# Kernel tuning notes

Measured on AMD Instinct MI355X. Metric: run time of the kernel, lower is better.

## Reference

```python
import jax, jax.numpy as jnp
import numpy as np

B, N, K, H = 8, 2048, 30, 128
SCALE = 30.0
EPS = 1e-5


def _gelu(x):
    return jax.nn.gelu(x, approximate=False)


def _lin(x, w, b):
    return x @ w.T + b


def _ln(x, g, b):
    m = x.mean(-1, keepdims=True)
    v = ((x - m) ** 2).mean(-1, keepdims=True)
    return g * (x - m) * jax.lax.rsqrt(v + EPS) + b


def _gather_nodes(h_V, E_idx):
    # h_V: [B,N,H], E_idx: [B,N,K] -> [B,N,K,H]
    b_idx = jnp.arange(h_V.shape[0])[:, None, None]
    return h_V[b_idx, E_idx]


def setup_inputs() -> dict:
    key = jax.random.key(0)
    ks = jax.random.split(key, 16)
    p = 0.02
    inp = {
        'h_V': jax.random.normal(ks[0], (B, N, H), jnp.float32),
        'h_E': jax.random.normal(ks[1], (B, N, K, H), jnp.float32),
        'E_idx': jax.random.randint(ks[2], (B, N, K), 0, N, jnp.int32),
        'mask_V': jnp.ones((B, N), jnp.float32),
        'mask_attend': jnp.ones((B, N, K), jnp.float32),
        # node message MLP (3H -> H -> H -> H)
        'W1_w': jax.random.normal(ks[3], (H, 3 * H), jnp.float32) * p,
        'W1_b': jnp.zeros((H,), jnp.float32),
        'W2_w': jax.random.normal(ks[4], (H, H), jnp.float32) * p,
        'W2_b': jnp.zeros((H,), jnp.float32),
        'W3_w': jax.random.normal(ks[5], (H, H), jnp.float32) * p,
        'W3_b': jnp.zeros((H,), jnp.float32),
        # edge message MLP (3H -> H -> H -> H)
        'W11_w': jax.random.normal(ks[6], (H, 3 * H), jnp.float32) * p,
        'W11_b': jnp.zeros((H,), jnp.float32),
        'W12_w': jax.random.normal(ks[7], (H, H), jnp.float32) * p,
        'W12_b': jnp.zeros((H,), jnp.float32),
        'W13_w': jax.random.normal(ks[8], (H, H), jnp.float32) * p,
        'W13_b': jnp.zeros((H,), jnp.float32),
        # layer norms
        'n1_g': jnp.ones((H,), jnp.float32), 'n1_b': jnp.zeros((H,), jnp.float32),
        'n2_g': jnp.ones((H,), jnp.float32), 'n2_b': jnp.zeros((H,), jnp.float32),
        'n3_g': jnp.ones((H,), jnp.float32), 'n3_b': jnp.zeros((H,), jnp.float32),
        # position-wise FFN (H -> 4H -> H)
        'din_w': jax.random.normal(ks[9], (4 * H, H), jnp.float32) * p,
        'din_b': jnp.zeros((4 * H,), jnp.float32),
        'dout_w': jax.random.normal(ks[10], (H, 4 * H), jnp.float32) * p,
        'dout_b': jnp.zeros((H,), jnp.float32),
    }
    return inp


def reference(h_V, h_E, E_idx, mask_V, mask_attend,
              W1_w, W1_b, W2_w, W2_b, W3_w, W3_b,
              W11_w, W11_b, W12_w, W12_b, W13_w, W13_b,
              n1_g, n1_b, n2_g, n2_b, n3_g, n3_b,
              din_w, din_b, dout_w, dout_b):
    k = h_E.shape[-2]
    # --- node update ---
    h_nbr = _gather_nodes(h_V, E_idx)                       # [B,N,K,H]
    h_V_exp = jnp.broadcast_to(h_V[:, :, None, :], h_nbr.shape)
    h_EV = jnp.concatenate([h_V_exp, h_nbr, h_E], axis=-1)  # [B,N,K,3H]
    h_message = _lin(_gelu(_lin(_gelu(_lin(h_EV, W1_w, W1_b)), W2_w, W2_b)), W3_w, W3_b)
    h_message = mask_attend[..., None] * h_message
    dh = jnp.sum(h_message, axis=-2) / SCALE
    h_V = _ln(h_V + dh, n1_g, n1_b)
    dh = _lin(_gelu(_lin(h_V, din_w, din_b)), dout_w, dout_b)
    h_V = _ln(h_V + dh, n2_g, n2_b)
    h_V = mask_V[..., None] * h_V
    # --- edge update ---
    h_nbr = _gather_nodes(h_V, E_idx)
    h_V_exp = jnp.broadcast_to(h_V[:, :, None, :], h_nbr.shape)
    h_EV = jnp.concatenate([h_V_exp, h_nbr, h_E], axis=-1)
    h_message = _lin(_gelu(_lin(_gelu(_lin(h_EV, W11_w, W11_b)), W12_w, W12_b)), W13_w, W13_b)
    h_E = _ln(h_E + h_message, n3_g, n3_b)
    return (h_V, h_E)
```

## Files before the change

### kernel.cpp

```cpp
#include <hip/hip_runtime.h>

#define B_ 8
#define N_ 2048
#define K_ 30
#define H_ 128
#define LDA 136
#define LDM 132
#define EPS_ 1e-5f

typedef __attribute__((ext_vector_type(8))) short short8;
typedef __attribute__((ext_vector_type(4))) float f32x4;

__device__ inline unsigned pkbf(float lo, float hi) {
  unsigned r;
  asm("v_cvt_pk_bf16_f32 %0, %1, %2" : "=v"(r) : "v"(lo), "v"(hi));
  return r;
}

__device__ inline unsigned short f2bf(float f) { return (unsigned short)pkbf(f, f); }

__device__ inline float bf2f(unsigned short h) {
  union { unsigned u; float f; } v; v.u = ((unsigned)h) << 16; return v.f;
}

__device__ inline float gelu_t(float x) {
  const float p = x * x;
  const float z = x * (1.5957691216057308f + 0.07135481627f * p);
  const float e = exp2f(z * -1.4426950408889634f);
  return x * __builtin_amdgcn_rcpf(1.0f + e);
}

__device__ inline short8 pack8(float4 a, float4 b) {
  union { unsigned u[4]; short8 s; } v;
  v.u[0] = pkbf(a.x, a.y); v.u[1] = pkbf(a.z, a.w);
  v.u[2] = pkbf(b.x, b.y); v.u[3] = pkbf(b.z, b.w);
  return v.s;
}

template<int LDW>
__device__ inline void gemmT(const unsigned short* __restrict__ sA,
                             const unsigned short* __restrict__ W,
                             int lane, int cb, f32x4 (&acc)[4][2]) {
  const int rl = lane & 15;
  const int klo = (lane >> 4) << 3;
#pragma unroll
  for (int ks = 0; ks < 4; ++ks) {
    short8 wf[2];
#pragma unroll
    for (int fn = 0; fn < 2; ++fn)
      wf[fn] = *(const short8*)(W + (size_t)(cb + fn * 16 + rl) * LDW + ks * 32 + klo);
#pragma unroll
    for (int et = 0; et < 4; ++et) {
      const short8 ef = *(const short8*)(sA + (et * 16 + rl) * LDA + ks * 32 + klo);
      acc[et][0] = __builtin_amdgcn_mfma_f32_16x16x32_bf16(wf[0], ef, acc[et][0], 0, 0, 0);
      acc[et][1] = __builtin_amdgcn_mfma_f32_16x16x32_bf16(wf[1], ef, acc[et][1], 0, 0, 0);
    }
  }
}

#define ZERO42(A) \
  _Pragma("unroll") for (int e_ = 0; e_ < 4; ++e_) { A[e_][0] = (f32x4){0,0,0,0}; A[e_][1] = (f32x4){0,0,0,0}; }

template<int LDW, int NN>
__device__ inline void gemm64(const unsigned short* __restrict__ sA,
                              const unsigned short* __restrict__ W,
                              int lane, int cb, f32x4 (&acc)[4][NN]) {
  const int rl = lane & 15;
  const int klo = (lane >> 4) << 3;
#pragma unroll
  for (int ks = 0; ks < 4; ++ks) {
    short8 a[4];
#pragma unroll
    for (int m = 0; m < 4; ++m)
      a[m] = *(const short8*)(sA + (m * 16 + rl) * LDA + ks * 32 + klo);
#pragma unroll
    for (int n = 0; n < NN; ++n) {
      const short8 b8 = *(const short8*)(W + (size_t)(cb + n * 16 + rl) * LDW + ks * 32 + klo);
#pragma unroll
      for (int m = 0; m < 4; ++m)
        acc[m][n] = __builtin_amdgcn_mfma_f32_16x16x32_bf16(a[m], b8, acc[m][n], 0, 0, 0);
    }
  }
}

__global__ __launch_bounds__(256) void prep(const float* __restrict__ w1, const float* __restrict__ w2,
                                            const float* __restrict__ w3, const float* __restrict__ w11,
                                            const float* __restrict__ w12, const float* __restrict__ w13,
                                            const float* __restrict__ din, const float* __restrict__ dout,
                                            unsigned short* __restrict__ dst) {
  const int i = blockIdx.x * 256 + threadIdx.x;
  const float* s; int off;
  if (i < 49152)       { s = w1;  off = 0; }
  else if (i < 65536)  { s = w2;  off = 49152; }
  else if (i < 81920)  { s = w3;  off = 65536; }
  else if (i < 131072) { s = w11; off = 81920; }
  else if (i < 147456) { s = w12; off = 131072; }
  else if (i < 163840) { s = w13; off = 147456; }
  else if (i < 229376) { s = din; off = 163840; }
  else                 { s = dout; off = 229376; }
  dst[i] = f2bf(s[i - off]);
}

template<bool F32SRC, bool SPLIT>
__global__ __launch_bounds__(256) void preY(const void* __restrict__ Xv,
                                            const unsigned short* __restrict__ Wbase,
                                            unsigned short* __restrict__ Yc,
                                            unsigned short* __restrict__ Yn) {
  __shared__ __align__(16) unsigned short sA[64 * LDA];
  const int tid = threadIdx.x;
  const int lane = tid & 63;
  const int w = tid >> 6;
  const int rows = blockIdx.x << 6;
  const int rl = lane & 15;
  const int h4 = (lane >> 4) << 2;

  if (F32SRC) {
    const float* X = (const float*)Xv;
    for (int t = tid; t < 1024; t += 256) {
      const int r = t >> 4, seg = t & 15;
      const float* src = X + (((size_t)(rows + r)) << 7) + seg * 8;
      *(short8*)(sA + r * LDA + seg * 8) = pack8(*(const float4*)src, *(const float4*)(src + 4));
    }
  } else {
    const unsigned short* X = (const unsigned short*)Xv;
    for (int t = tid; t < 1024; t += 256) {
      const int r = t >> 4, seg = t & 15;
      *(short8*)(sA + r * LDA + seg * 8) =
          *(const short8*)(X + (((size_t)(rows + r)) << 7) + seg * 8);
    }
  }
  __syncthreads();

  const int half = w >> 1;
  const int cb = (w & 1) * 64;
  f32x4 acc[4][4];
#pragma unroll
  for (int m = 0; m < 4; ++m)
#pragma unroll
    for (int n = 0; n < 4; ++n) acc[m][n] = (f32x4){0, 0, 0, 0};
  gemm64<384, 4>(sA, Wbase + half * 128, lane, cb, acc);

  unsigned short* Y = half ? Yn : Yc;
  const int stride = SPLIT ? 128 : 256;
  const int coff = SPLIT ? 0 : half * 128;
#pragma unroll
  for (int n = 0; n < 4; ++n) {
    const int col = coff + cb + n * 16 + rl;
#pragma unroll
    for (int m = 0; m < 4; ++m)
#pragma unroll
      for (int i = 0; i < 4; ++i)
        Y[(size_t)(rows + m * 16 + h4 + i) * stride + col] = f2bf(acc[m][n][i]);
  }
}

__global__ __launch_bounds__(256, 4) void k1(
    const float* __restrict__ hV, const float* __restrict__ hE,
    const int* __restrict__ Eidx, const float* __restrict__ mattend,
    const unsigned short* __restrict__ wc, const unsigned short* __restrict__ Y1,
    const float* __restrict__ W1b, const float* __restrict__ W2b,
    const float* __restrict__ W3b, const float* __restrict__ n1g,
    const float* __restrict__ n1b, unsigned short* __restrict__ hV1b,
    float* __restrict__ outE) {
  __shared__ __align__(16) unsigned short sBuf[2 * 64 * LDA];
  __shared__ __align__(16) unsigned short sYc[2 * 128];
  __shared__ float sMask[64];
  __shared__ float sRed[2][128];
  unsigned short* sE = sBuf;
  unsigned short* sG = sBuf + 64 * LDA;
  float* sM = (float*)sBuf;

  const int tid = threadIdx.x;
  const int lane = tid & 63;
  const int w = tid >> 6;
  const int rl = lane & 15;
  const int h4 = (lane >> 4) << 2;
  const int bid = (blockIdx.x & 7) * 1024 + (blockIdx.x >> 3);
  const int v0 = bid << 1;
  const int b = v0 >> 11;
  const int n0 = v0 & (N_ - 1);
  const int bBase = b * N_;

  const unsigned short* W1c = wc;
  const unsigned short* W2c = wc + 49152;
  const unsigned short* W3c = wc + 65536;

  for (int t = tid; t < 1024; t += 256) {
    const int r = t >> 4, seg = t & 15;
    const int g = r >> 5, kk = r & 31;
    const int kc = kk < K_ ? kk : K_ - 1;
    const size_t e = (size_t)(bBase + n0 + g) * K_ + kc;
    const float* src = hE + (e << 7) + seg * 8;
    const short8 o = pack8(*(const float4*)src, *(const float4*)(src + 4));
    *(short8*)(sE + r * LDA + seg * 8) = o;
    if (kk < K_)
      *(short8*)((unsigned short*)(outE + (e << 7)) + 128 + seg * 8) = o;
  }
  for (int t = tid; t < 1024; t += 256) {
    const int r = t >> 4, seg = t & 15;
    const int g = r >> 5;
    int kk = r & 31; if (kk >= K_) kk = K_ - 1;
    const int j = Eidx[(bBase + n0 + g) * K_ + kk];
    *(short8*)(sG + r * LDA + seg * 8) =
        *(const short8*)(Y1 + (size_t)(bBase + j) * 256 + 128 + seg * 8);
  }
  {
    const int g = tid >> 7, c = tid & 127;
    sYc[g * 128 + c] = Y1[(size_t)(bBase + n0 + g) * 256 + c];
  }
  if (tid < 64) {
    const int g = tid >> 5, kk = tid & 31;
    sMask[tid] = (kk < K_) ? mattend[(bBase + n0 + g) * K_ + kk] : 0.f;
  }
  __syncthreads();

  f32x4 acc[4][2];
  ZERO42(acc)
  gemmT<384>(sE, W1c + 256, lane, w * 32, acc);

  {
    float4 b1v[2];
    b1v[0] = *(const float4*)(W1b + w * 32 + h4);
    b1v[1] = *(const float4*)(W1b + w * 32 + 16 + h4);
#pragma unroll
    for (int et = 0; et < 4; ++et) {
      const int e = et * 16 + rl;
      const int g = et >> 1;
#pragma unroll
      for (int fn = 0; fn < 2; ++fn) {
        const int f0 = w * 32 + fn * 16 + h4;
        const ushort4 yc = *(const ushort4*)(sYc + g * 128 + f0);
        const ushort4 yn = *(const ushort4*)(sG + e * LDA + f0);
        const float x0 = gelu_t(acc[et][fn][0] + b1v[fn].x + bf2f(yc.x) + bf2f(yn.x));
        const float x1 = gelu_t(acc[et][fn][1] + b1v[fn].y + bf2f(yc.y) + bf2f(yn.y));
        const float x2 = gelu_t(acc[et][fn][2] + b1v[fn].z + bf2f(yc.z) + bf2f(yn.z));
        const float x3 = gelu_t(acc[et][fn][3] + b1v[fn].w + bf2f(yc.w) + bf2f(yn.w));
        uint2 o; o.x = pkbf(x0, x1); o.y = pkbf(x2, x3);
        *(uint2*)(sG + e * LDA + f0) = o;
      }
    }
  }
  __syncthreads();

  f32x4 acc2[4][2];
  ZERO42(acc2)
  gemmT<128>(sG, W2c, lane, w * 32, acc2);
  __syncthreads();
  {
    float4 b2v[2];
    b2v[0] = *(const float4*)(W2b + w * 32 + h4);
    b2v[1] = *(const float4*)(W2b + w * 32 + 16 + h4);
#pragma unroll
    for (int et = 0; et < 4; ++et) {
      const int e = et * 16 + rl;
#pragma unroll
      for (int fn = 0; fn < 2; ++fn) {
        const int f0 = w * 32 + fn * 16 + h4;
        const float x0 = gelu_t(acc2[et][fn][0] + b2v[fn].x);
        const float x1 = gelu_t(acc2[et][fn][1] + b2v[fn].y);
        const float x2 = gelu_t(acc2[et][fn][2] + b2v[fn].z);
        const float x3 = gelu_t(acc2[et][fn][3] + b2v[fn].w);
        uint2 o; o.x = pkbf(x0, x1); o.y = pkbf(x2, x3);
        *(uint2*)(sG + e * LDA + f0) = o;
      }
    }
  }
  __syncthreads();

  f32x4 acc3[4][2];
  ZERO42(acc3)
  gemmT<128>(sG, W3c, lane, w * 32, acc3);
  __syncthreads();

  {
    float4 b3v[2];
    b3v[0] = *(const float4*)(W3b + w * 32 + h4);
    b3v[1] = *(const float4*)(W3b + w * 32 + 16 + h4);
#pragma unroll
    for (int et = 0; et < 4; ++et) {
      const int e = et * 16 + rl;
      const float mk = sMask[e];
#pragma unroll
      for (int fn = 0; fn < 2; ++fn) {
        const int f0 = w * 32 + fn * 16 + h4;
        const float4 v = make_float4((acc3[et][fn][0] + b3v[fn].x) * mk,
                                     (acc3[et][fn][1] + b3v[fn].y) * mk,
                                     (acc3[et][fn][2] + b3v[fn].z) * mk,
                                     (acc3[et][fn][3] + b3v[fn].w) * mk);
        *(float4*)(sM + e * LDM + f0) = v;
      }
    }
  }
  __syncthreads();

  {
    const int g = tid >> 7, f = tid & 127;
    float s = 0.f;
#pragma unroll
    for (int kk = 0; kk < 32; ++kk) s += sM[(g * 32 + kk) * LDM + f];
    sRed[g][f] = s;
  }
  __syncthreads();

  if (w < 2) {
    const size_t base = ((size_t)(bBase + n0 + w)) << 7;
    const float x0 = hV[base + lane] + sRed[w][lane] * (1.0f / 30.0f);
    const float x1 = hV[base + 64 + lane] + sRed[w][64 + lane] * (1.0f / 30.0f);
    float s = x0 + x1;
#pragma unroll
    for (int o = 1; o < 64; o <<= 1) s += __shfl_xor(s, o);
    const float mean = s * (1.0f / 128.0f);
    const float d0 = x0 - mean, d1 = x1 - mean;
    float vs = d0 * d0 + d1 * d1;
#pragma unroll
    for (int o = 1; o < 64; o <<= 1) vs += __shfl_xor(vs, o);
    const float inv = rsqrtf(vs * (1.0f / 128.0f) + EPS_);
    hV1b[base + lane] = f2bf(n1g[lane] * (d0 * inv) + n1b[lane]);
    hV1b[base + 64 + lane] = f2bf(n1g[64 + lane] * (d1 * inv) + n1b[64 + lane]);
  }
}

__global__ __launch_bounds__(256) void k2(
    const unsigned short* __restrict__ hV1b, const unsigned short* __restrict__ wc,
    const float* __restrict__ dinb, const float* __restrict__ doutb,
    const float* __restrict__ n2g, const float* __restrict__ n2b,
    const float* __restrict__ maskV, float* __restrict__ outV,
    unsigned short* __restrict__ hV2c) {
  __shared__ __align__(16) unsigned short sT[16 * LDA];
  __shared__ float sStat[16][2][4];

  const int tid = threadIdx.x;
  const int lane = tid & 63;
  const int w = tid >> 6;
  const int rl = lane & 15;
  const int h4 = (lane >> 4) << 2;
  const int klo = (lane >> 4) << 3;
  const int rowbase = blockIdx.x << 4;

  const unsigned short* dinc = wc + 163840;
  const unsigned short* doutc = wc + 229376;

  short8 ef[4];
#pragma unroll
  for (int ks = 0; ks < 4; ++ks)
    ef[ks] = *(const short8*)(hV1b + (((size_t)(rowbase + rl)) << 7) + ks * 32 + klo);

  f32x4 acc2[2];
  acc2[0] = (f32x4){0, 0, 0, 0}; acc2[1] = (f32x4){0, 0, 0, 0};

  for (int c = 0; c < 4; ++c) {
    f32x4 acc1[2];
    acc1[0] = (f32x4){0, 0, 0, 0}; acc1[1] = (f32x4){0, 0, 0, 0};
#pragma unroll
    for (int ks = 0; ks < 4; ++ks)
#pragma unroll
      for (int fn = 0; fn < 2; ++fn) {
        const short8 wf = *(const short8*)(dinc + (size_t)(c * 128 + w * 32 + fn * 16 + rl) * 128 + ks * 32 + klo);
        acc1[fn] = __builtin_amdgcn_mfma_f32_16x16x32_bf16(wf, ef[ks], acc1[fn], 0, 0, 0);
      }
    __syncthreads();
    {
      float4 db[2];
      db[0] = *(const float4*)(dinb + c * 128 + w * 32 + h4);
      db[1] = *(const float4*)(dinb + c * 128 + w * 32 + 16 + h4);
#pragma unroll
      for (int fn = 0; fn < 2; ++fn) {
        const int f0 = w * 32 + fn * 16 + h4;
        const float x0 = gelu_t(acc1[fn][0] + db[fn].x);
        const float x1 = gelu_t(acc1[fn][1] + db[fn].y);
        const float x2 = gelu_t(acc1[fn][2] + db[fn].z);
        const float x3 = gelu_t(acc1[fn][3] + db[fn].w);
        uint2 o; o.x = pkbf(x0, x1); o.y = pkbf(x2, x3);
        *(uint2*)(sT + rl * LDA + f0) = o;
      }
    }
    __syncthreads();
#pragma unroll
    for (int ks = 0; ks < 4; ++ks) {
      const short8 xf = *(const short8*)(sT + rl * LDA + ks * 32 + klo);
#pragma unroll
      for (int fn = 0; fn < 2; ++fn) {
        const short8 wf2 = *(const short8*)(doutc + (size_t)(w * 32 + fn * 16 + rl) * 512 + c * 128 + ks * 32 + klo);
        acc2[fn] = __builtin_amdgcn_mfma_f32_16x16x32_bf16(wf2, xf, acc2[fn], 0, 0, 0);
      }
    }
  }

  const int row = rl;
  const int grow = rowbase + row;
  {
    float4 wbv[2];
    wbv[0] = *(const float4*)(doutb + w * 32 + h4);
    wbv[1] = *(const float4*)(doutb + w * 32 + 16 + h4);
    float s = 0.f, ss = 0.f;
#pragma unroll
    for (int fn = 0; fn < 2; ++fn) {
      const int f0 = w * 32 + fn * 16 + h4;
      const ushort4 rr = *(const ushort4*)(hV1b + (((size_t)grow) << 7) + f0);
      const float x0 = acc2[fn][0] + wbv[fn].x + bf2f(rr.x);
      const float x1 = acc2[fn][1] + wbv[fn].y + bf2f(rr.y);
      const float x2 = acc2[fn][2] + wbv[fn].z + bf2f(rr.z);
      const float x3 = acc2[fn][3] + wbv[fn].w + bf2f(rr.w);
      acc2[fn] = (f32x4){x0, x1, x2, x3};
      s += x0 + x1 + x2 + x3;
      ss += x0 * x0 + x1 * x1 + x2 * x2 + x3 * x3;
    }
    s += __shfl_xor(s, 16); s += __shfl_xor(s, 32);
    ss += __shfl_xor(ss, 16); ss += __shfl_xor(ss, 32);
    if (lane < 16) { sStat[row][0][w] = s; sStat[row][1][w] = ss; }
  }
  __syncthreads();
  {
    const float sum = sStat[row][0][0] + sStat[row][0][1] + sStat[row][0][2] + sStat[row][0][3];
    const float ssq = sStat[row][1][0] + sStat[row][1][1] + sStat[row][1][2] + sStat[row][1][3];
    const float mean = sum * (1.0f / 128.0f);
    const float inv = rsqrtf(ssq * (1.0f / 128.0f) - mean * mean + EPS_);
    const float mv = maskV[grow];
#pragma unroll
    for (int fn = 0; fn < 2; ++fn) {
      const int f0 = w * 32 + fn * 16 + h4;
      const float4 gv = *(const float4*)(n2g + f0);
      const float4 bv = *(const float4*)(n2b + f0);
      const float y0 = (gv.x * (acc2[fn][0] - mean) * inv + bv.x) * mv;
      const float y1 = (gv.y * (acc2[fn][1] - mean) * inv + bv.y) * mv;
      const float y2 = (gv.z * (acc2[fn][2] - mean) * inv + bv.z) * mv;
      const float y3 = (gv.w * (acc2[fn][3] - mean) * inv + bv.w) * mv;
      *(float4*)(outV + (((size_t)grow) << 7) + f0) = make_float4(y0, y1, y2, y3);
      uint2 o; o.x = pkbf(y0, y1); o.y = pkbf(y2, y3);
      *(uint2*)(hV2c + (((size_t)grow) << 7) + f0) = o;
    }
  }
}

__global__ __launch_bounds__(256, 4) void k3(
    const int* __restrict__ Eidx, const unsigned short* __restrict__ wc,
    const unsigned short* __restrict__ Y2c, const unsigned short* __restrict__ Y2n,
    const float* __restrict__ W11b, const float* __restrict__ W12b,
    const float* __restrict__ W13b, const float* __restrict__ n3g,
    const float* __restrict__ n3b, float* __restrict__ outE) {
  __shared__ __align__(16) unsigned short sE[64 * LDA];
  __shared__ __align__(16) unsigned short sG[64 * LDA];
  __shared__ unsigned short sYc[2 * 128];
  __shared__ float sStat[64][2][4];

  const int tid = threadIdx.x;
  const int lane = tid & 63;
  const int w = tid >> 6;
  const int rl = lane & 15;
  const int h4 = (lane >> 4) << 2;
  const int bid = (blockIdx.x & 7) * 1024 + (blockIdx.x >> 3);
  const int v0 = bid << 1;
  const int b = v0 >> 11;
  const int n0 = v0 & (N_ - 1);
  const int bBase = b * N_;

  const unsigned short* W11c = wc + 81920;
  const unsigned short* W12c = wc + 131072;
  const unsigned short* W13c = wc + 147456;

  for (int t = tid; t < 1024; t += 256) {
    const int r = t >> 4, seg = t & 15;
    const int g = r >> 5;
    int kk = r & 31; if (kk >= K_) kk = K_ - 1;
    const size_t e = (size_t)(bBase + n0 + g) * K_ + kk;
    *(short8*)(sE + r * LDA + seg * 8) =
        *(const short8*)((const unsigned short*)(outE + (e << 7)) + 128 + seg * 8);
  }
  for (int t = tid; t < 1024; t += 256) {
    const int r = t >> 4, seg = t & 15;
    const int g = r >> 5;
    int kk = r & 31; if (kk >= K_) kk = K_ - 1;
    const int j = Eidx[(bBase + n0 + g) * K_ + kk];
    *(short8*)(sG + r * LDA + seg * 8) =
        *(const short8*)(Y2n + (size_t)(bBase + j) * 128 + seg * 8);
  }
  {
    const int g = tid >> 7, c = tid & 127;
    sYc[g * 128 + c] = Y2c[(size_t)(bBase + n0 + g) * 128 + c];
  }
  __syncthreads();

  f32x4 acc[4][2];
  ZERO42(acc)
  gemm64<384, 2>(sE, W11c + 256, lane, w * 32, acc);

#pragma unroll
  for (int n = 0; n < 2; ++n) {
    const int f = w * 32 + n * 16 + rl;
    const float bb = W11b[f];
#pragma unroll
    for (int m = 0; m < 4; ++m)
#pragma unroll
      for (int i = 0; i < 4; ++i) {
        const int e = m * 16 + h4 + i;
        const float x = acc[m][n][i] + bb + bf2f(sYc[(e >> 5) * 128 + f]) + bf2f(sG[e * LDA + f]);
        sG[e * LDA + f] = f2bf(gelu_t(x));
      }
  }
  __syncthreads();

  f32x4 acc2[4][2];
  ZERO42(acc2)
  gemm64<128, 2>(sG, W12c, lane, w * 32, acc2);
  __syncthreads();
#pragma unroll
  for (int n = 0; n < 2; ++n) {
    const int f = w * 32 + n * 16 + rl;
    const float bb = W12b[f];
#pragma unroll
    for (int m = 0; m < 4; ++m)
#pragma unroll
      for (int i = 0; i < 4; ++i) {
        const int e = m * 16 + h4 + i;
        sG[e * LDA + f] = f2bf(gelu_t(acc2[m][n][i] + bb));
      }
  }
  __syncthreads();

  f32x4 acc3[4][2];
  ZERO42(acc3)
  gemm64<128, 2>(sG, W13c, lane, w * 32, acc3);

  float gc[2], bc[2], wb[2];
#pragma unroll
  for (int n = 0; n < 2; ++n) {
    const int f = w * 32 + n * 16 + rl;
    gc[n] = n3g[f]; bc[n] = n3b[f]; wb[n] = W13b[f];
  }
#pragma unroll
  for (int m = 0; m < 4; ++m)
#pragma unroll
    for (int i = 0; i < 4; ++i) {
      const int e = m * 16 + h4 + i;
      float s = 0.f, ss = 0.f;
#pragma unroll
      for (int n = 0; n < 2; ++n) {
        const int f = w * 32 + n * 16 + rl;
        const float x = acc3[m][n][i] + wb[n] + bf2f(sE[e * LDA + f]);
        acc3[m][n][i] = x;
        s += x; ss += x * x;
      }
#pragma unroll
      for (int o = 1; o <= 8; o <<= 1) { s += __shfl_xor(s, o); ss += __shfl_xor(ss, o); }
      if (rl == 0) { sStat[e][0][w] = s; sStat[e][1][w] = ss; }
    }
  __syncthreads();
#pragma unroll
  for (int m = 0; m < 4; ++m)
#pragma unroll
    for (int i = 0; i < 4; ++i) {
      const int e = m * 16 + h4 + i;
      const int g = e >> 5, kk = e & 31;
      if (kk >= K_) continue;
      const float sum = sStat[e][0][0] + sStat[e][0][1] + sStat[e][0][2] + sStat[e][0][3];
      const float ssq = sStat[e][1][0] + sStat[e][1][1] + sStat[e][1][2] + sStat[e][1][3];
      const float mean = sum * (1.0f / 128.0f);
      const float inv = rsqrtf(ssq * (1.0f / 128.0f) - mean * mean + EPS_);
      float* dst = outE + (((size_t)((bBase + n0 + g) * K_ + kk)) << 7) + w * 32 + rl;
#pragma unroll
      for (int n = 0; n < 2; ++n)
        dst[n * 16] = gc[n] * (acc3[m][n][i] - mean) * inv + bc[n];
    }
}

extern "C" void kernel_launch(void* const* d_in, const int* in_sizes, int n_in,
                              void* d_out, int out_size, void* d_ws, size_t ws_size,
                              hipStream_t stream) {
  const float* hV = (const float*)d_in[0];
  const float* hE = (const float*)d_in[1];
  const int* Eidx = (const int*)d_in[2];
  const float* maskV = (const float*)d_in[3];
  const float* mattend = (const float*)d_in[4];
  const float* W1w = (const float*)d_in[5];   const float* W1b = (const float*)d_in[6];
  const float* W2w = (const float*)d_in[7];   const float* W2b = (const float*)d_in[8];
  const float* W3w = (const float*)d_in[9];   const float* W3b = (const float*)d_in[10];
  const float* W11w = (const float*)d_in[11]; const float* W11b = (const float*)d_in[12];
  const float* W12w = (const float*)d_in[13]; const float* W12b = (const float*)d_in[14];
  const float* W13w = (const float*)d_in[15]; const float* W13b = (const float*)d_in[16];
  const float* n1g = (const float*)d_in[17];  const float* n1b = (const float*)d_in[18];
  const float* n2g = (const float*)d_in[19];  const float* n2b = (const float*)d_in[20];
  const float* n3g = (const float*)d_in[21];  const float* n3b = (const float*)d_in[22];
  const float* dinw = (const float*)d_in[23]; const float* dinb = (const float*)d_in[24];
  const float* doutw = (const float*)d_in[25]; const float* doutb = (const float*)d_in[26];

  unsigned short* wc   = (unsigned short*)d_ws;
  unsigned short* R1   = wc + 294912;
  unsigned short* R2   = R1 + 4194304;
  unsigned short* Y1   = R1;
  unsigned short* hV1b = R2;
  unsigned short* hV2c = R1;
  unsigned short* Y2c  = R1 + 2097152;
  unsigned short* Y2n  = R2;

  float* outV = (float*)d_out;
  float* outE = outV + (size_t)B_ * N_ * H_;

  prep<<<1152, 256, 0, stream>>>(W1w, W2w, W3w, W11w, W12w, W13w, dinw, doutw, wc);
  preY<true, false><<<256, 256, 0, stream>>>(hV, wc, Y1, Y1);
  k1<<<8192, 256, 0, stream>>>(hV, hE, Eidx, mattend, wc, Y1,
                               W1b, W2b, W3b, n1g, n1b, hV1b, outE);
  k2<<<1024, 256, 0, stream>>>(hV1b, wc, dinb, doutb, n2g, n2b, maskV, outV, hV2c);
  preY<false, true><<<256, 256, 0, stream>>>(hV2c, wc + 81920, Y2c, Y2n);
  k3<<<8192, 256, 0, stream>>>(Eidx, wc, Y2c, Y2n,
                               W11b, W12b, W13b, n3g, n3b, outE);
}
```

Baseline: 457.9 us.

## Process one node per block with two waves in edge MLP kernels

k1 and k3 now handle one node (32 padded edge rows) per 128-thread block instead of two nodes per 256-thread block. Each wave computes 64 output features across 32 rows with new gemmT1/gemm32 tiles, and the LayerNorm and reduction bookkeeping is simplified to match. The aim is to cut shared memory per block and raise the number of resident blocks for better latency hiding. In exchange, each block spends more of its time on fixed setup and barriers, and weight fragments are reused across fewer rows.

After: 570.9 us. +24.7%, slower.

```diff
diff --git a/kernel.cpp b/kernel.cpp
--- a/kernel.cpp
+++ b/kernel.cpp
@@ -38,28 +38,48 @@
 }
 
 template<int LDW>
-__device__ inline void gemmT(const unsigned short* __restrict__ sA,
-                             const unsigned short* __restrict__ W,
-                             int lane, int cb, f32x4 (&acc)[4][2]) {
+__device__ inline void gemmT1(const unsigned short* __restrict__ sA,
+                              const unsigned short* __restrict__ W,
+                              int lane, int cb, f32x4 (&acc)[2][4]) {
   const int rl = lane & 15;
   const int klo = (lane >> 4) << 3;
 #pragma unroll
   for (int ks = 0; ks < 4; ++ks) {
-    short8 wf[2];
-#pragma unroll
-    for (int fn = 0; fn < 2; ++fn)
+    short8 wf[4];
+#pragma unroll
+    for (int fn = 0; fn < 4; ++fn)
       wf[fn] = *(const short8*)(W + (size_t)(cb + fn * 16 + rl) * LDW + ks * 32 + klo);
 #pragma unroll
-    for (int et = 0; et < 4; ++et) {
+    for (int et = 0; et < 2; ++et) {
       const short8 ef = *(const short8*)(sA + (et * 16 + rl) * LDA + ks * 32 + klo);
-      acc[et][0] = __builtin_amdgcn_mfma_f32_16x16x32_bf16(wf[0], ef, acc[et][0], 0, 0, 0);
-      acc[et][1] = __builtin_amdgcn_mfma_f32_16x16x32_bf16(wf[1], ef, acc[et][1], 0, 0, 0);
-    }
-  }
-}
-
-#define ZERO42(A) \
-  _Pragma("unroll") for (int e_ = 0; e_ < 4; ++e_) { A[e_][0] = (f32x4){0,0,0,0}; A[e_][1] = (f32x4){0,0,0,0}; }
+#pragma unroll
+      for (int fn = 0; fn < 4; ++fn)
+        acc[et][fn] = __builtin_amdgcn_mfma_f32_16x16x32_bf16(wf[fn], ef, acc[et][fn], 0, 0, 0);
+    }
+  }
+}
+
+template<int LDW>
+__device__ inline void gemm32(const unsigned short* __restrict__ sA,
+                              const unsigned short* __restrict__ W,
+                              int lane, int cb, f32x4 (&acc)[2][4]) {
+  const int rl = lane & 15;
+  const int klo = (lane >> 4) << 3;
+#pragma unroll
+  for (int ks = 0; ks < 4; ++ks) {
+    short8 a[2];
+#pragma unroll
+    for (int m = 0; m < 2; ++m)
+      a[m] = *(const short8*)(sA + (m * 16 + rl) * LDA + ks * 32 + klo);
+#pragma unroll
+    for (int n = 0; n < 4; ++n) {
+      const short8 b8 = *(const short8*)(W + (size_t)(cb + n * 16 + rl) * LDW + ks * 32 + klo);
+#pragma unroll
+      for (int m = 0; m < 2; ++m)
+        acc[m][n] = __builtin_amdgcn_mfma_f32_16x16x32_bf16(a[m], b8, acc[m][n], 0, 0, 0);
+    }
+  }
+}
 
 template<int LDW, int NN>
 __device__ inline void gemm64(const unsigned short* __restrict__ sA,
@@ -82,6 +102,10 @@
     }
   }
 }
+
+#define ZERO24(A) \
+  _Pragma("unroll") for (int e_ = 0; e_ < 2; ++e_) \
+  _Pragma("unroll") for (int f_ = 0; f_ < 4; ++f_) A[e_][f_] = (f32x4){0.f, 0.f, 0.f, 0.f};
 
 __global__ __launch_bounds__(256) void prep(const float* __restrict__ w1, const float* __restrict__ w2,
                                             const float* __restrict__ w3, const float* __restrict__ w11,
@@ -154,7 +178,7 @@
   }
 }
 
-__global__ __launch_bounds__(256, 4) void k1(
+__global__ __launch_bounds__(128, 4) void k1(
     const float* __restrict__ hV, const float* __restrict__ hE,
     const int* __restrict__ Eidx, const float* __restrict__ mattend,
     const unsigned short* __restrict__ wc, const unsigned short* __restrict__ Y1,
@@ -162,12 +186,12 @@
     const float* __restrict__ W3b, const float* __restrict__ n1g,
     const float* __restrict__ n1b, unsigned short* __restrict__ hV1b,
     float* __restrict__ outE) {
-  __shared__ __align__(16) unsigned short sBuf[2 * 64 * LDA];
-  __shared__ __align__(16) unsigned short sYc[2 * 128];
-  __shared__ float sMask[64];
-  __shared__ float sRed[2][128];
+  __shared__ __align__(16) unsigned short sBuf[2 * 32 * LDA];
+  __shared__ __align__(16) unsigned short sYc[128];
+  __shared__ float sMask[32];
+  __shared__ float sRed[128];
   unsigned short* sE = sBuf;
-  unsigned short* sG = sBuf + 64 * LDA;
+  unsigned short* sG = sBuf + 32 * LDA;
   float* sM = (float*)sBuf;
 
   const int tid = threadIdx.x;
@@ -175,61 +199,52 @@
   const int w = tid >> 6;
   const int rl = lane & 15;
   const int h4 = (lane >> 4) << 2;
-  const int bid = (blockIdx.x & 7) * 1024 + (blockIdx.x >> 3);
-  const int v0 = bid << 1;
-  const int b = v0 >> 11;
-  const int n0 = v0 & (N_ - 1);
+  const int bid = (blockIdx.x & 7) * 2048 + (blockIdx.x >> 3);
+  const int b = bid >> 11;
+  const int n0 = bid & (N_ - 1);
   const int bBase = b * N_;
+  const int node = bBase + n0;
 
   const unsigned short* W1c = wc;
   const unsigned short* W2c = wc + 49152;
   const unsigned short* W3c = wc + 65536;
 
-  for (int t = tid; t < 1024; t += 256) {
+  for (int t = tid; t < 512; t += 128) {
     const int r = t >> 4, seg = t & 15;
-    const int g = r >> 5, kk = r & 31;
-    const int kc = kk < K_ ? kk : K_ - 1;
-    const size_t e = (size_t)(bBase + n0 + g) * K_ + kc;
+    const int kc = r < K_ ? r : K_ - 1;
+    const size_t e = (size_t)node * K_ + kc;
     const float* src = hE + (e << 7) + seg * 8;
     const short8 o = pack8(*(const float4*)src, *(const float4*)(src + 4));
     *(short8*)(sE + r * LDA + seg * 8) = o;
-    if (kk < K_)
+    if (r < K_)
       *(short8*)((unsigned short*)(outE + (e << 7)) + 128 + seg * 8) = o;
   }
-  for (int t = tid; t < 1024; t += 256) {
+  for (int t = tid; t < 512; t += 128) {
     const int r = t >> 4, seg = t & 15;
-    const int g = r >> 5;
-    int kk = r & 31; if (kk >= K_) kk = K_ - 1;
-    const int j = Eidx[(bBase + n0 + g) * K_ + kk];
+    const int kc = r < K_ ? r : K_ - 1;
+    const int j = Eidx[node * K_ + kc];
     *(short8*)(sG + r * LDA + seg * 8) =
         *(const short8*)(Y1 + (size_t)(bBase + j) * 256 + 128 + seg * 8);
   }
+  sYc[tid] = Y1[(size_t)node * 256 + tid];
+  if (tid < 32) sMask[tid] = (tid < K_) ? mattend[node * K_ + tid] : 0.f;
+  __syncthreads();
+
+  f32x4 acc[2][4];
+  ZERO24(acc)
+  gemmT1<384>(sE, W1c + 256, lane, w * 64, acc);
+
   {
-    const int g = tid >> 7, c = tid & 127;
-    sYc[g * 128 + c] = Y1[(size_t)(bBase + n0 + g) * 256 + c];
-  }
-  if (tid < 64) {
-    const int g = tid >> 5, kk = tid & 31;
-    sMask[tid] = (kk < K_) ? mattend[(bBase + n0 + g) * K_ + kk] : 0.f;
-  }
-  __syncthreads();
-
-  f32x4 acc[4][2];
-  ZERO42(acc)
-  gemmT<384>(sE, W1c + 256, lane, w * 32, acc);
-
-  {
-    float4 b1v[2];
-    b1v[0] = *(const float4*)(W1b + w * 32 + h4);
-    b1v[1] = *(const float4*)(W1b + w * 32 + 16 + h4);
-#pragma unroll
-    for (int et = 0; et < 4; ++et) {
+    float4 b1v[4];
+#pragma unroll
+    for (int fn = 0; fn < 4; ++fn) b1v[fn] = *(const float4*)(W1b + w * 64 + fn * 16 + h4);
+#pragma unroll
+    for (int et = 0; et < 2; ++et) {
       const int e = et * 16 + rl;
-      const int g = et >> 1;
-#pragma unroll
-      for (int fn = 0; fn < 2; ++fn) {
-        const int f0 = w * 32 + fn * 16 + h4;
-        const ushort4 yc = *(const ushort4*)(sYc + g * 128 + f0);
+#pragma unroll
+      for (int fn = 0; fn < 4; ++fn) {
+        const int f0 = w * 64 + fn * 16 + h4;
+        const ushort4 yc = *(const ushort4*)(sYc + f0);
         const ushort4 yn = *(const ushort4*)(sG + e * LDA + f0);
         const float x0 = gelu_t(acc[et][fn][0] + b1v[fn].x + bf2f(yc.x) + bf2f(yn.x));
         const float x1 = gelu_t(acc[et][fn][1] + b1v[fn].y + bf2f(yc.y) + bf2f(yn.y));
@@ -242,20 +257,20 @@
   }
   __syncthreads();
 
-  f32x4 acc2[4][2];
-  ZERO42(acc2)
-  gemmT<128>(sG, W2c, lane, w * 32, acc2);
+  f32x4 acc2[2][4];
+  ZERO24(acc2)
+  gemmT1<128>(sG, W2c, lane, w * 64, acc2);
   __syncthreads();
   {
-    float4 b2v[2];
-    b2v[0] = *(const float4*)(W2b + w * 32 + h4);
-    b2v[1] = *(const float4*)(W2b + w * 32 + 16 + h4);
-#pragma unroll
-    for (int et = 0; et < 4; ++et) {
+    float4 b2v[4];
+#pragma unroll
+    for (int fn = 0; fn < 4; ++fn) b2v[fn] = *(const float4*)(W2b + w * 64 + fn * 16 + h4);
+#pragma unroll
+    for (int et = 0; et < 2; ++et) {
       const int e = et * 16 + rl;
 #pragma unroll
-      for (int fn = 0; fn < 2; ++fn) {
-        const int f0 = w * 32 + fn * 16 + h4;
+      for (int fn = 0; fn < 4; ++fn) {
+        const int f0 = w * 64 + fn * 16 + h4;
         const float x0 = gelu_t(acc2[et][fn][0] + b2v[fn].x);
         const float x1 = gelu_t(acc2[et][fn][1] + b2v[fn].y);
         const float x2 = gelu_t(acc2[et][fn][2] + b2v[fn].z);
@@ -267,22 +282,22 @@
   }
   __syncthreads();
 
-  f32x4 acc3[4][2];
-  ZERO42(acc3)
-  gemmT<128>(sG, W3c, lane, w * 32, acc3);
+  f32x4 acc3[2][4];
+  ZERO24(acc3)
+  gemmT1<128>(sG, W3c, lane, w * 64, acc3);
   __syncthreads();
 
   {
-    float4 b3v[2];
-    b3v[0] = *(const float4*)(W3b + w * 32 + h4);
-    b3v[1] = *(const float4*)(W3b + w * 32 + 16 + h4);
-#pragma unroll
-    for (int et = 0; et < 4; ++et) {
+    float4 b3v[4];
+#pragma unroll
+    for (int fn = 0; fn < 4; ++fn) b3v[fn] = *(const float4*)(W3b + w * 64 + fn * 16 + h4);
+#pragma unroll
+    for (int et = 0; et < 2; ++et) {
       const int e = et * 16 + rl;
       const float mk = sMask[e];
 #pragma unroll
-      for (int fn = 0; fn < 2; ++fn) {
-        const int f0 = w * 32 + fn * 16 + h4;
+      for (int fn = 0; fn < 4; ++fn) {
+        const int f0 = w * 64 + fn * 16 + h4;
         const float4 v = make_float4((acc3[et][fn][0] + b3v[fn].x) * mk,
                                      (acc3[et][fn][1] + b3v[fn].y) * mk,
                                      (acc3[et][fn][2] + b3v[fn].z) * mk,
@@ -294,18 +309,17 @@
   __syncthreads();
 
   {
-    const int g = tid >> 7, f = tid & 127;
     float s = 0.f;
 #pragma unroll
-    for (int kk = 0; kk < 32; ++kk) s += sM[(g * 32 + kk) * LDM + f];
-    sRed[g][f] = s;
-  }
-  __syncthreads();
-
-  if (w < 2) {
-    const size_t base = ((size_t)(bBase + n0 + w)) << 7;
-    const float x0 = hV[base + lane] + sRed[w][lane] * (1.0f / 30.0f);
-    const float x1 = hV[base + 64 + lane] + sRed[w][64 + lane] * (1.0f / 30.0f);
+    for (int kk = 0; kk < 32; ++kk) s += sM[kk * LDM + tid];
+    sRed[tid] = s;
+  }
+  __syncthreads();
+
+  if (w == 0) {
+    const size_t base = ((size_t)node) << 7;
+    const float x0 = hV[base + lane] + sRed[lane] * (1.0f / 30.0f);
+    const float x1 = hV[base + 64 + lane] + sRed[64 + lane] * (1.0f / 30.0f);
     float s = x0 + x1;
 #pragma unroll
     for (int o = 1; o < 64; o <<= 1) s += __shfl_xor(s, o);
@@ -432,83 +446,79 @@
   }
 }
 
-__global__ __launch_bounds__(256, 4) void k3(
+__global__ __launch_bounds__(128, 4) void k3(
     const int* __restrict__ Eidx, const unsigned short* __restrict__ wc,
     const unsigned short* __restrict__ Y2c, const unsigned short* __restrict__ Y2n,
     const float* __restrict__ W11b, const float* __restrict__ W12b,
     const float* __restrict__ W13b, const float* __restrict__ n3g,
     const float* __restrict__ n3b, float* __restrict__ outE) {
-  __shared__ __align__(16) unsigned short sE[64 * LDA];
-  __shared__ __align__(16) unsigned short sG[64 * LDA];
-  __shared__ unsigned short sYc[2 * 128];
-  __shared__ float sStat[64][2][4];
+  __shared__ __align__(16) unsigned short sE[32 * LDA];
+  __shared__ __align__(16) unsigned short sG[32 * LDA];
+  __shared__ unsigned short sYc[128];
+  __shared__ float sStat[32][2][2];
 
   const int tid = threadIdx.x;
   const int lane = tid & 63;
   const int w = tid >> 6;
   const int rl = lane & 15;
   const int h4 = (lane >> 4) << 2;
-  const int bid = (blockIdx.x & 7) * 1024 + (blockIdx.x >> 3);
-  const int v0 = bid << 1;
-  const int b = v0 >> 11;
-  const int n0 = v0 & (N_ - 1);
+  const int bid = (blockIdx.x & 7) * 2048 + (blockIdx.x >> 3);
+  const int b = bid >> 11;
+  const int n0 = bid & (N_ - 1);
   const int bBase = b * N_;
+  const int node = bBase + n0;
 
   const unsigned short* W11c = wc + 81920;
   const unsigned short* W12c = wc + 131072;
   const unsigned short* W13c = wc + 147456;
 
-  for (int t = tid; t < 1024; t += 256) {
+  for (int t = tid; t < 512; t += 128) {
     const int r = t >> 4, seg = t & 15;
-    const int g = r >> 5;
-    int kk = r & 31; if (kk >= K_) kk = K_ - 1;
-    const size_t e = (size_t)(bBase + n0 + g) * K_ + kk;
+    const int kc = r < K_ ? r : K_ - 1;
+    const size_t e = (size_t)node * K_ + kc;
     *(short8*)(sE + r * LDA + seg * 8) =
         *(const short8*)((const unsigned short*)(outE + (e << 7)) + 128 + seg * 8);
   }
-  for (int t = tid; t < 1024; t += 256) {
+  for (int t = tid; t < 512; t += 128) {
     const int r = t >> 4, seg = t & 15;
-    const int g = r >> 5;
-    int kk = r & 31; if (kk >= K_) kk = K_ - 1;
-    const int j = Eidx[(bBase + n0 + g) * K_ + kk];
+    const int kc = r < K_ ? r : K_ - 1;
+    const int j = Eidx[node * K_ + kc];
     *(short8*)(sG + r * LDA + seg * 8) =
         *(const short8*)(Y2n + (size_t)(bBase + j) * 128 + seg * 8);
   }
-  {
-    const int g = tid >> 7, c = tid & 127;
-    sYc[g * 128 + c] = Y2c[(size_t)(bBase + n0 + g) * 128 + c];
-  }
-  __syncthreads();
-
-  f32x4 acc[4][2];
-  ZERO42(acc)
-  gemm64<384, 2>(sE, W11c + 256, lane, w * 32, acc);
-
-#pragma unroll
-  for (int n = 0; n < 2; ++n) {
-    const int f = w * 32 + n * 16 + rl;
+  sYc[tid] = Y2c[(size_t)node * 128 + tid];
+  __syncthreads();
+
+  f32x4 acc[2][4];
+  ZERO24(acc)
+  gemm32<384>(sE, W11c + 256, lane, w * 64, acc);
+
+#pragma unroll
+  for (int n = 0; n < 4; ++n) {
+    const int f = w * 64 + n * 16 + rl;
     const float bb = W11b[f];
-#pragma unroll
-    for (int m = 0; m < 4; ++m)
+    const float yc = bf2f(sYc[f]);
+#pragma unroll
+    for (int m = 0; m < 2; ++m)
 #pragma unroll
       for (int i = 0; i < 4; ++i) {
         const int e = m * 16 + h4 + i;
-        const float x = acc[m][n][i] + bb + bf2f(sYc[(e >> 5) * 128 + f]) + bf2f(sG[e * LDA + f]);
+        const float x = acc[m][n][i] + bb + yc + bf2f(sG[e * LDA + f]);
         sG[e * LDA + f] = f2bf(gelu_t(x));
       }
   }
   __syncthreads();
 
-  f32x4 acc2[4][2];
-  ZERO42(acc2)
-  gemm64<128, 2>(sG, W12c, lane, w * 32, acc2);
-  __syncthreads();
-#pragma unroll
-  for (int n = 0; n < 2; ++n) {
-    const int f = w * 32 + n * 16 + rl;
+  f32x4 acc2[2][4];
+  ZERO24(acc2)
+  gemm32<128>(sG, W12c, lane, w * 64, acc2);
+  __syncthreads();
+#pragma unroll
+  for (int n = 0; n < 4; ++n) {
+    const int f = w * 64 + n * 16 + rl;
     const float bb = W12b[f];
 #pragma unroll
-    for (int m = 0; m < 4; ++m)
+    for (int m = 0; m < 2; ++m)
 #pragma unroll
       for (int i = 0; i < 4; ++i) {
         const int e = m * 16 + h4 + i;
@@ -517,25 +527,25 @@
   }
   __syncthreads();
 
-  f32x4 acc3[4][2];
-  ZERO42(acc3)
-  gemm64<128, 2>(sG, W13c, lane, w * 32, acc3);
-
-  float gc[2], bc[2], wb[2];
-#pragma unroll
-  for (int n = 0; n < 2; ++n) {
-    const int f = w * 32 + n * 16 + rl;
+  f32x4 acc3[2][4];
+  ZERO24(acc3)
+  gemm32<128>(sG, W13c, lane, w * 64, acc3);
+
+  float gc[4], bc[4], wb[4];
+#pragma unroll
+  for (int n = 0; n < 4; ++n) {
+    const int f = w * 64 + n * 16 + rl;
     gc[n] = n3g[f]; bc[n] = n3b[f]; wb[n] = W13b[f];
   }
 #pragma unroll
-  for (int m = 0; m < 4; ++m)
+  for (int m = 0; m < 2; ++m)
 #pragma unroll
     for (int i = 0; i < 4; ++i) {
       const int e = m * 16 + h4 + i;
       float s = 0.f, ss = 0.f;
 #pragma unroll
-      for (int n = 0; n < 2; ++n) {
-        const int f = w * 32 + n * 16 + rl;
+      for (int n = 0; n < 4; ++n) {
+        const int f = w * 64 + n * 16 + rl;
         const float x = acc3[m][n][i] + wb[n] + bf2f(sE[e * LDA + f]);
         acc3[m][n][i] = x;
         s += x; ss += x * x;
@@ -546,19 +556,18 @@
     }
   __syncthreads();
 #pragma unroll
-  for (int m = 0; m < 4; ++m)
+  for (int m = 0; m < 2; ++m)
 #pragma unroll
     for (int i = 0; i < 4; ++i) {
       const int e = m * 16 + h4 + i;
-      const int g = e >> 5, kk = e & 31;
-      if (kk >= K_) continue;
-      const float sum = sStat[e][0][0] + sStat[e][0][1] + sStat[e][0][2] + sStat[e][0][3];
-      const float ssq = sStat[e][1][0] + sStat[e][1][1] + sStat[e][1][2] + sStat[e][1][3];
+      if (e >= K_) continue;
+      const float sum = sStat[e][0][0] + sStat[e][0][1];
+      const float ssq = sStat[e][1][0] + sStat[e][1][1];
       const float mean = sum * (1.0f / 128.0f);
       const float inv = rsqrtf(ssq * (1.0f / 128.0f) - mean * mean + EPS_);
-      float* dst = outE + (((size_t)((bBase + n0 + g) * K_ + kk)) << 7) + w * 32 + rl;
-#pragma unroll
-      for (int n = 0; n < 2; ++n)
+      float* dst = outE + (((size_t)(node * K_ + e)) << 7) + w * 64 + rl;
+#pragma unroll
+      for (int n = 0; n < 4; ++n)
         dst[n * 16] = gc[n] * (acc3[m][n][i] - mean) * inv + bc[n];
     }
 }
@@ -597,10 +606,10 @@
 
   prep<<<1152, 256, 0, stream>>>(W1w, W2w, W3w, W11w, W12w, W13w, dinw, doutw, wc);
   preY<true, false><<<256, 256, 0, stream>>>(hV, wc, Y1, Y1);
-  k1<<<8192, 256, 0, stream>>>(hV, hE, Eidx, mattend, wc, Y1,
-                               W1b, W2b, W3b, n1g, n1b, hV1b, outE);
+  k1<<<16384, 128, 0, stream>>>(hV, hE, Eidx, mattend, wc, Y1,
+                                W1b, W2b, W3b, n1g, n1b, hV1b, outE);
   k2<<<1024, 256, 0, stream>>>(hV1b, wc, dinb, doutb, n2g, n2b, maskV, outV, hV2c);
   preY<false, true><<<256, 256, 0, stream>>>(hV2c, wc + 81920, Y2c, Y2n);
-  k3<<<8192, 256, 0, stream>>>(Eidx, wc, Y2c, Y2n,
-                               W11b, W12b, W13b, n3g, n3b, outE);
-}
+  k3<<<16384, 128, 0, stream>>>(Eidx, wc, Y2c, Y2n,
+                                W11b, W12b, W13b, n3g, n3b, outE);
+}
```
